# Performance work log

Hardware: AMD Instinct MI355X
Metric: run time of the kernel (lower is better)

## Reference

```python
import jax, jax.numpy as jnp
import numpy as np

DIM = 2048
B, T = 8, 2048


def _layernorm(x, g, b, eps=1e-5):
    m = jnp.mean(x, axis=-1, keepdims=True)
    v = jnp.mean(jnp.square(x - m), axis=-1, keepdims=True)
    return (x - m) / jnp.sqrt(v + eps) * g + b


def _shift(x):
    # token shift: x_prev[t] = x[t-1], x_prev[0] = 0 (zero initial state)
    return jnp.pad(x[:, :-1, :], ((0, 0), (1, 0), (0, 0)))


def setup_inputs() -> dict:
    key = jax.random.key(0)
    ks = jax.random.split(key, 16)
    d = DIM
    s = 0.02  # init scale for weight matrices
    inp = {
        "x": jax.random.normal(ks[0], (B, T, d), dtype=jnp.float32),
        "ln1_g": jnp.ones((d,), jnp.float32),
        "ln1_b": jnp.zeros((d,), jnp.float32),
        "ln2_g": jnp.ones((d,), jnp.float32),
        "ln2_b": jnp.zeros((d,), jnp.float32),
        # time-mix params (w,u init to zeros as in source)
        "tm_w": jnp.zeros((d,), jnp.float32),
        "tm_u": jnp.zeros((d,), jnp.float32),
        "tm_mu_r": jax.random.uniform(ks[1], (d,), jnp.float32),
        "tm_mu_k": jax.random.uniform(ks[2], (d,), jnp.float32),
        "tm_mu_v": jax.random.uniform(ks[3], (d,), jnp.float32),
        "tm_Wr": jax.random.normal(ks[4], (d, d), jnp.float32) * s,
        "tm_Wk": jax.random.normal(ks[5], (d, d), jnp.float32) * s,
        "tm_Wv": jax.random.normal(ks[6], (d, d), jnp.float32) * s,
        "tm_Wout": jax.random.normal(ks[7], (d, d), jnp.float32) * s,
        # channel-mix params
        "cm_mu_r": jax.random.uniform(ks[8], (d,), jnp.float32),
        "cm_mu_k": jax.random.uniform(ks[9], (d,), jnp.float32),
        "cm_Wr": jax.random.normal(ks[10], (d, d), jnp.float32) * s,
        "cm_Wk": jax.random.normal(ks[11], (d, d), jnp.float32) * s,
        "cm_Wv": jax.random.normal(ks[12], (d, d), jnp.float32) * s,
    }
    return inp


def reference(x, ln1_g, ln1_b, ln2_g, ln2_b, tm_w, tm_u, tm_mu_r, tm_mu_k,
              tm_mu_v, tm_Wr, tm_Wk, tm_Wv, tm_Wout, cm_mu_r, cm_mu_k,
              cm_Wr, cm_Wk, cm_Wv):
    # ---- time mixing (after ln1) ----
    h = _layernorm(x, ln1_g, ln1_b)
    hp = _shift(h)
    xr = tm_mu_r * h + (1.0 - tm_mu_r) * hp
    xk = tm_mu_k * h + (1.0 - tm_mu_k) * hp
    xv = tm_mu_v * h + (1.0 - tm_mu_v) * hp
    r = jax.nn.sigmoid(jnp.einsum('btc,dc->btd', xr, tm_Wr))
    k = jnp.einsum('btc,dc->btd', xk, tm_Wk)
    v = jnp.einsum('btc,dc->btd', xv, tm_Wv)
    # NOTE: in the source, state a,b are decayed each step but never
    # accumulated with exp(k)*v; with zero initial state they remain 0,
    # so num = exp(u+k)*v, den = exp(u+k). This reproduces that exactly.
    ek = jnp.exp(tm_u + k)
    wkv = (ek * v) / (ek + 1e-8)
    x = x + jnp.einsum('btc,dc->btd', r * wkv, tm_Wout)

    # ---- channel mixing (after ln2) ----
    h2 = _layernorm(x, ln2_g, ln2_b)
    h2p = _shift(h2)
    xr2 = cm_mu_r * h2 + (1.0 - cm_mu_r) * h2p
    xk2 = cm_mu_k * h2 + (1.0 - cm_mu_k) * h2p
    r2 = jax.nn.sigmoid(jnp.einsum('btc,dc->btd', xr2, cm_Wr))
    k2 = jnp.square(jax.nn.relu(jnp.einsum('btc,dc->btd', xk2, cm_Wk)))
    x = x + r2 * jnp.einsum('btc,dc->btd', k2, cm_Wv)
    return x
```

## Files before the change

### kernel.cpp

```cpp
#include <hip/hip_runtime.h>
#include <cstdint>

typedef __attribute__((ext_vector_type(8))) short bf16x8;
typedef __attribute__((ext_vector_type(4))) float f32x4;
typedef unsigned short u16;

__device__ __forceinline__ u16 f2bf(float f) {
  unsigned u = __float_as_uint(f);
  u += 0x7FFFu + ((u >> 16) & 1u);
  return (u16)(u >> 16);
}
__device__ __forceinline__ float bf2f(u16 h) {
  return __uint_as_float(((unsigned)h) << 16);
}
__device__ __forceinline__ ushort4 pack4(float4 v) {
  return make_ushort4(f2bf(v.x), f2bf(v.y), f2bf(v.z), f2bf(v.w));
}
__device__ __forceinline__ void gload16(const void* g, void* lds) {
  __builtin_amdgcn_global_load_lds(
      (__attribute__((address_space(1))) void*)g,
      (__attribute__((address_space(3))) void*)lds, 16, 0, 0);
}

template<int MODE>
__global__ __launch_bounds__(256)
void gemm2048(const u16* __restrict__ A, const u16* __restrict__ W,
              u16* oB, float* oF, const u16* aux1, const float* auxF)
{
  __shared__ u16 As[128 * 32];
  __shared__ u16 Ws[128 * 32];
  const int tid  = threadIdx.x;
  const int lane = tid & 63;
  const int wave = tid >> 6;
  const int wr = wave >> 1, wc = wave & 1;
  const int lrow = lane & 15, quad = lane >> 4;
  const long bm = (long)blockIdx.x * 128;
  const long bn = (long)blockIdx.y * 128;

  f32x4 acc[4][4] = {};

  const u16* Ag = A + bm * 2048;
  const u16* Wg = W + bn * 2048;

  for (int k0 = 0; k0 < 2048; k0 += 32) {
    __syncthreads();
#pragma unroll
    for (int p = 0; p < 2; ++p) {
      const int row = p * 64 + (tid >> 2);
      const int col = (tid & 3) * 8;
      const int lb  = p * 2048 + (tid & 192) * 8;
      gload16(Ag + (long)row * 2048 + k0 + col, &As[lb]);
      gload16(Wg + (long)row * 2048 + k0 + col, &Ws[lb]);
    }
    __syncthreads();

    bf16x8 af[4], wf[4];
#pragma unroll
    for (int t = 0; t < 4; ++t) {
      af[t] = *(const bf16x8*)&As[(wr * 64 + t * 16 + lrow) * 32 + quad * 8];
      wf[t] = *(const bf16x8*)&Ws[(wc * 64 + t * 16 + lrow) * 32 + quad * 8];
    }
#pragma unroll
    for (int mi = 0; mi < 4; ++mi)
#pragma unroll
      for (int ni = 0; ni < 4; ++ni)
        acc[mi][ni] = __builtin_amdgcn_mfma_f32_16x16x32_bf16(af[mi], wf[ni], acc[mi][ni], 0, 0, 0);
  }

#pragma unroll
  for (int mi = 0; mi < 4; ++mi) {
    const long gm = bm + wr * 64 + mi * 16 + quad * 4;
#pragma unroll
    for (int ni = 0; ni < 4; ++ni) {
      const long gn = bn + wc * 64 + ni * 16 + lrow;
#pragma unroll
      for (int i = 0; i < 4; ++i) {
        const long idx = (gm + i) * 2048 + gn;
        const float a = acc[mi][ni][i];
        if constexpr (MODE == 1) {
          oB[idx] = f2bf(1.f / (1.f + __expf(-a)));
        } else if constexpr (MODE == 2) {
          oB[idx] = f2bf(bf2f(aux1[idx]) * a);
        } else if constexpr (MODE == 3) {
          oF[idx] = auxF[idx] + a;
        } else if constexpr (MODE == 4) {
          const float t = fmaxf(a, 0.f);
          oB[idx] = f2bf(t * t);
        } else {
          oF[idx] = oF[idx] + bf2f(aux1[idx]) * a;
        }
      }
    }
  }
}

__device__ __forceinline__ float sum4(float4 v) { return v.x + v.y + v.z + v.w; }
__device__ __forceinline__ float sumsq4(float4 v) { return v.x*v.x + v.y*v.y + v.z*v.z + v.w*v.w; }
__device__ __forceinline__ float4 ln4(float4 x, float m, float r, float4 g, float4 b) {
  return make_float4((x.x-m)*r*g.x+b.x, (x.y-m)*r*g.y+b.y, (x.z-m)*r*g.z+b.z, (x.w-m)*r*g.w+b.w);
}
__device__ __forceinline__ float4 mix4(float4 mu, float4 h, float4 hp) {
  return make_float4(mu.x*h.x + (1.f-mu.x)*hp.x, mu.y*h.y + (1.f-mu.y)*hp.y,
                     mu.z*h.z + (1.f-mu.z)*hp.z, mu.w*h.w + (1.f-mu.w)*hp.w);
}
__device__ __forceinline__ float4 scl4(float4 v, float s) {
  return make_float4(v.x*s, v.y*s, v.z*s, v.w*s);
}

__global__ __launch_bounds__(256)
void ln_mix(const float* __restrict__ X, const float* __restrict__ g,
            const float* __restrict__ b, const float* __restrict__ mua,
            const float* __restrict__ mub,
            u16* __restrict__ o_a, u16* __restrict__ o_b)
{
  const int tid = threadIdx.x;
  const long row = blockIdx.x;
  const bool hasp = (row & 2047) != 0;
  const float* xc = X + row * 2048;
  const float* xp = xc - 2048;

  const float4 c0 = ((const float4*)xc)[tid];
  const float4 c1 = ((const float4*)xc)[tid + 256];
  float4 p0 = make_float4(0.f, 0.f, 0.f, 0.f), p1 = p0;
  if (hasp) { p0 = ((const float4*)xp)[tid]; p1 = ((const float4*)xp)[tid + 256]; }

  float sc = sum4(c0) + sum4(c1), qc = sumsq4(c0) + sumsq4(c1);
  float sp = sum4(p0) + sum4(p1), qp = sumsq4(p0) + sumsq4(p1);
#pragma unroll
  for (int off = 32; off > 0; off >>= 1) {
    sc += __shfl_down(sc, off);
    qc += __shfl_down(qc, off);
    sp += __shfl_down(sp, off);
    qp += __shfl_down(qp, off);
  }
  __shared__ float red[4][4];
  const int wave = tid >> 6, lane = tid & 63;
  if (lane == 0) { red[wave][0] = sc; red[wave][1] = qc; red[wave][2] = sp; red[wave][3] = qp; }
  __syncthreads();
  sc = red[0][0] + red[1][0] + red[2][0] + red[3][0];
  qc = red[0][1] + red[1][1] + red[2][1] + red[3][1];
  sp = red[0][2] + red[1][2] + red[2][2] + red[3][2];
  qp = red[0][3] + red[1][3] + red[2][3] + red[3][3];

  const float inv = 1.f / 2048.f;
  const float mc = sc * inv;
  const float rc = rsqrtf(fmaxf(qc * inv - mc * mc, 0.f) + 1e-5f);
  const float mp = sp * inv;
  const float rp = rsqrtf(fmaxf(qp * inv - mp * mp, 0.f) + 1e-5f);
  const float wp = hasp ? 1.f : 0.f;

  const float4 g0 = ((const float4*)g)[tid], g1 = ((const float4*)g)[tid + 256];
  const float4 b0 = ((const float4*)b)[tid], b1 = ((const float4*)b)[tid + 256];

  const float4 h0 = ln4(c0, mc, rc, g0, b0), h1 = ln4(c1, mc, rc, g1, b1);
  const float4 hp0 = scl4(ln4(p0, mp, rp, g0, b0), wp);
  const float4 hp1 = scl4(ln4(p1, mp, rp, g1, b1), wp);

  const long ro = row * 2048;
  {
    const float4 m0 = ((const float4*)mua)[tid], m1 = ((const float4*)mua)[tid + 256];
    ((ushort4*)(o_a + ro))[tid]       = pack4(mix4(m0, h0, hp0));
    ((ushort4*)(o_a + ro))[tid + 256] = pack4(mix4(m1, h1, hp1));
  }
  {
    const float4 m0 = ((const float4*)mub)[tid], m1 = ((const float4*)mub)[tid + 256];
    ((ushort4*)(o_b + ro))[tid]       = pack4(mix4(m0, h0, hp0));
    ((ushort4*)(o_b + ro))[tid + 256] = pack4(mix4(m1, h1, hp1));
  }
}

__global__ __launch_bounds__(256)
void cvt_w(const float* w0, const float* w1, const float* w2, const float* w3,
           const float* w4, const float* w5, u16* dst)
{
  const int i = blockIdx.x * 256 + threadIdx.x;
  const int seg = i >> 20;
  const int off = i & 1048575;
  const float* src;
  switch (seg) {
    case 0: src = w0; break; case 1: src = w1; break; case 2: src = w2; break;
    case 3: src = w3; break; case 4: src = w4; break;
    default: src = w5; break;
  }
  const float4 v = ((const float4*)src)[off];
  ((ushort4*)dst)[i] = pack4(v);
}

extern "C" void kernel_launch(void* const* d_in, const int* in_sizes, int n_in,
                              void* d_out, int out_size, void* d_ws, size_t ws_size,
                              hipStream_t stream)
{
  (void)in_sizes; (void)n_in; (void)out_size; (void)ws_size;
  const float* x    = (const float*)d_in[0];
  const float* ln1g = (const float*)d_in[1];
  const float* ln1b = (const float*)d_in[2];
  const float* ln2g = (const float*)d_in[3];
  const float* ln2b = (const float*)d_in[4];
  const float* tmur = (const float*)d_in[7];
  const float* tmuv = (const float*)d_in[9];
  const float* Wr   = (const float*)d_in[10];
  const float* Wv   = (const float*)d_in[12];
  const float* Wout = (const float*)d_in[13];
  const float* cmur = (const float*)d_in[14];
  const float* cmuk = (const float*)d_in[15];
  const float* cWr  = (const float*)d_in[16];
  const float* cWk  = (const float*)d_in[17];
  const float* cWv  = (const float*)d_in[18];
  float* out = (float*)d_out;

  char* ws = (char*)d_ws;
  u16* Wb = (u16*)ws;
  u16* xa = (u16*)(ws + 50331648L);
  u16* xb = (u16*)(ws + 117440512L);
  u16* rb = (u16*)(ws + 184549376L);
  u16* kb = (u16*)(ws + 251658240L);
  u16* WrB   = Wb;
  u16* WvB   = Wb + 1L * 4194304;
  u16* WoutB = Wb + 2L * 4194304;
  u16* cWrB  = Wb + 3L * 4194304;
  u16* cWkB  = Wb + 4L * 4194304;
  u16* cWvB  = Wb + 5L * 4194304;

  const dim3 gG(128, 16), blk(256);

  cvt_w<<<24576, blk, 0, stream>>>(Wr, Wv, Wout, cWr, cWk, cWv, Wb);
  ln_mix<<<16384, blk, 0, stream>>>(x, ln1g, ln1b, tmur, tmuv, xa, xb);
  gemm2048<1><<<gG, blk, 0, stream>>>(xa, WrB, rb, nullptr, nullptr, nullptr);
  gemm2048<2><<<gG, blk, 0, stream>>>(xb, WvB, rb, nullptr, rb, nullptr);
  gemm2048<3><<<gG, blk, 0, stream>>>(rb, WoutB, nullptr, out, nullptr, x);
  ln_mix<<<16384, blk, 0, stream>>>(out, ln2g, ln2b, cmur, cmuk, xa, xb);
  gemm2048<1><<<gG, blk, 0, stream>>>(xa, cWrB, rb, nullptr, nullptr, nullptr);
  gemm2048<4><<<gG, blk, 0, stream>>>(xb, cWkB, kb, nullptr, nullptr, nullptr);
  gemm2048<5><<<gG, blk, 0, stream>>>(kb, cWvB, nullptr, out, rb, nullptr);
}
```

Baseline: 1.714 ms.

## Rewrite GEMM as 256x256-tile, 8-wave kernel with multi-stage async LDS pipeline

```diff
diff --git a/kernel.cpp b/kernel.cpp
--- a/kernel.cpp
+++ b/kernel.cpp
@@ -23,56 +23,76 @@
 }
 
 template<int MODE>
-__global__ __launch_bounds__(256)
+__global__ __launch_bounds__(512, 2)
 void gemm2048(const u16* __restrict__ A, const u16* __restrict__ W,
               u16* oB, float* oF, const u16* aux1, const float* auxF)
 {
-  __shared__ u16 As[128 * 32];
-  __shared__ u16 Ws[128 * 32];
+  __shared__ u16 lds[2][2][2][16][512];
   const int tid  = threadIdx.x;
   const int lane = tid & 63;
   const int wave = tid >> 6;
-  const int wr = wave >> 1, wc = wave & 1;
-  const int lrow = lane & 15, quad = lane >> 4;
-  const long bm = (long)blockIdx.x * 128;
-  const long bn = (long)blockIdx.y * 128;
-
-  f32x4 acc[4][4] = {};
+  const int wr = wave >> 2, wc = wave & 3;
+  const int l15 = lane & 15, lq = lane >> 4;
+  const long bm = (long)blockIdx.x * 256;
+  const long bn = (long)blockIdx.y * 256;
 
   const u16* Ag = A + bm * 2048;
   const u16* Wg = W + bn * 2048;
-
-  for (int k0 = 0; k0 < 2048; k0 += 32) {
-    __syncthreads();
-#pragma unroll
-    for (int p = 0; p < 2; ++p) {
-      const int row = p * 64 + (tid >> 2);
-      const int col = (tid & 3) * 8;
-      const int lb  = p * 2048 + (tid & 192) * 8;
-      gload16(Ag + (long)row * 2048 + k0 + col, &As[lb]);
-      gload16(Wg + (long)row * 2048 + k0 + col, &Ws[lb]);
-    }
-    __syncthreads();
-
-    bf16x8 af[4], wf[4];
-#pragma unroll
-    for (int t = 0; t < 4; ++t) {
-      af[t] = *(const bf16x8*)&As[(wr * 64 + t * 16 + lrow) * 32 + quad * 8];
-      wf[t] = *(const bf16x8*)&Ws[(wc * 64 + t * 16 + lrow) * 32 + quad * 8];
-    }
-#pragma unroll
-    for (int mi = 0; mi < 4; ++mi)
+  const long soff = (long)l15 * 2048 + lq * 8;
+  const int b0 = wave * 2, b1 = wave * 2 + 1;
+
+  f32x4 acc[8][4] = {};
+
+  auto STAGE = [&](int buf, int kt, int sk) {
+    const long kb = (long)kt * 64 + sk * 32;
+    gload16(Ag + (long)b0 * 32768 + soff + kb, &lds[buf][0][sk][b0][0]);
+    gload16(Wg + (long)b0 * 32768 + soff + kb, &lds[buf][1][sk][b0][0]);
+    gload16(Ag + (long)b1 * 32768 + soff + kb, &lds[buf][0][sk][b1][0]);
+    gload16(Wg + (long)b1 * 32768 + soff + kb, &lds[buf][1][sk][b1][0]);
+  };
+
+  auto COMPUTE = [&](int buf, int sk) {
+    bf16x8 af[8], bfr[4];
+#pragma unroll
+    for (int mi = 0; mi < 8; ++mi)
+      af[mi] = *(const bf16x8*)&lds[buf][0][sk][wr * 8 + mi][lane * 8];
+#pragma unroll
+    for (int ni = 0; ni < 4; ++ni)
+      bfr[ni] = *(const bf16x8*)&lds[buf][1][sk][wc * 4 + ni][lane * 8];
+    __builtin_amdgcn_s_setprio(1);
+#pragma unroll
+    for (int mi = 0; mi < 8; ++mi)
 #pragma unroll
       for (int ni = 0; ni < 4; ++ni)
-        acc[mi][ni] = __builtin_amdgcn_mfma_f32_16x16x32_bf16(af[mi], wf[ni], acc[mi][ni], 0, 0, 0);
-  }
-
-#pragma unroll
-  for (int mi = 0; mi < 4; ++mi) {
-    const long gm = bm + wr * 64 + mi * 16 + quad * 4;
+        acc[mi][ni] = __builtin_amdgcn_mfma_f32_16x16x32_bf16(af[mi], bfr[ni], acc[mi][ni], 0, 0, 0);
+    __builtin_amdgcn_s_setprio(0);
+  };
+
+#define WAITBAR(N) do {                                        \
+    asm volatile("s_waitcnt vmcnt(" #N ")" ::: "memory");      \
+    __builtin_amdgcn_s_barrier();                              \
+    asm volatile("" ::: "memory");                             \
+  } while (0)
+
+  STAGE(0, 0, 0); STAGE(0, 0, 1); STAGE(1, 1, 0);
+
+  for (int t = 0; t < 30; ++t) {
+    const int cur = t & 1;
+    WAITBAR(8); STAGE(cur ^ 1, t + 1, 1); COMPUTE(cur, 0);
+    WAITBAR(8); STAGE(cur, t + 2, 0);     COMPUTE(cur, 1);
+  }
+  WAITBAR(8); STAGE(1, 31, 1); COMPUTE(0, 0);
+  WAITBAR(8);                  COMPUTE(0, 1);
+  WAITBAR(4);                  COMPUTE(1, 0);
+  WAITBAR(0);                  COMPUTE(1, 1);
+#undef WAITBAR
+
+#pragma unroll
+  for (int mi = 0; mi < 8; ++mi) {
+    const long gm = bm + wr * 128 + mi * 16 + lq * 4;
 #pragma unroll
     for (int ni = 0; ni < 4; ++ni) {
-      const long gn = bn + wc * 64 + ni * 16 + lrow;
+      const long gn = bn + wc * 64 + ni * 16 + l15;
 #pragma unroll
       for (int i = 0; i < 4; ++i) {
         const long idx = (gm + i) * 2048 + gn;
@@ -221,15 +241,15 @@
   u16* cWkB  = Wb + 4L * 4194304;
   u16* cWvB  = Wb + 5L * 4194304;
 
-  const dim3 gG(128, 16), blk(256);
+  const dim3 gG(64, 8), blkG(512), blk(256);
 
   cvt_w<<<24576, blk, 0, stream>>>(Wr, Wv, Wout, cWr, cWk, cWv, Wb);
   ln_mix<<<16384, blk, 0, stream>>>(x, ln1g, ln1b, tmur, tmuv, xa, xb);
-  gemm2048<1><<<gG, blk, 0, stream>>>(xa, WrB, rb, nullptr, nullptr, nullptr);
-  gemm2048<2><<<gG, blk, 0, stream>>>(xb, WvB, rb, nullptr, rb, nullptr);
-  gemm2048<3><<<gG, blk, 0, stream>>>(rb, WoutB, nullptr, out, nullptr, x);
+  gemm2048<1><<<gG, blkG, 0, stream>>>(xa, WrB, rb, nullptr, nullptr, nullptr);
+  gemm2048<2><<<gG, blkG, 0, stream>>>(xb, WvB, rb, nullptr, rb, nullptr);
+  gemm2048<3><<<gG, blkG, 0, stream>>>(rb, WoutB, nullptr, out, nullptr, x);
   ln_mix<<<16384, blk, 0, stream>>>(out, ln2g, ln2b, cmur, cmuk, xa, xb);
-  gemm2048<1><<<gG, blk, 0, stream>>>(xa, cWrB, rb, nullptr, nullptr, nullptr);
-  gemm2048<4><<<gG, blk, 0, stream>>>(xb, cWkB, kb, nullptr, nullptr, nullptr);
-  gemm2048<5><<<gG, blk, 0, stream>>>(kb, cWvB, nullptr, out, rb, nullptr);
-}
+  gemm2048<1><<<gG, blkG, 0, stream>>>(xa, cWrB, rb, nullptr, nullptr, nullptr);
+  gemm2048<4><<<gG, blkG, 0, stream>>>(xb, cWkB, kb, nullptr, nullptr, nullptr);
+  gemm2048<5><<<gG, blkG, 0, stream>>>(kb, cWvB, nullptr, out, rb, nullptr);
+}
```

Measured after the change: 1.554 ms. 9.3% less time.
